# Kernel optimization log

Hardware: AMD Instinct MI355X
Metric: run time of the kernel (lower is better)

## Reference

```python
import jax, jax.numpy as jnp
import numpy as np

B, T, C, H = 1024, 256, 384, 64
NEG_INF = -1e30


def setup_inputs() -> dict:
    key = jax.random.key(0)
    kx, kk, kq, kv = jax.random.split(key, 4)
    return {
        "x": jax.random.normal(kx, (B, T, C), dtype=jnp.float32),
        "Wk": jax.random.normal(kk, (C, H), dtype=jnp.float32) * (C ** -0.5),
        "Wq": jax.random.normal(kq, (C, H), dtype=jnp.float32) * (C ** -0.5),
        "Wv": jax.random.normal(kv, (C, H), dtype=jnp.float32) * (C ** -0.5),
    }


def reference(x, Wk, Wq, Wv):
    # Single causal self-attention head (eval mode: dropout is identity).
    k = jnp.einsum("btc,ch->bth", x, Wk)  # [B,T,H]
    q = jnp.einsum("btc,ch->bth", x, Wq)
    v = jnp.einsum("btc,ch->bth", x, Wv)
    scale = jnp.asarray(k.shape[-1], x.dtype) ** -0.5
    w = jnp.einsum("bqh,bkh->bqk", q, k) * scale  # [B,T,T]
    Tn = x.shape[1]
    causal = jnp.tril(jnp.ones((Tn, Tn), dtype=bool))
    w = jnp.where(causal, w, NEG_INF)
    w = jax.nn.softmax(w, axis=-1)
    return jnp.einsum("bqk,bkh->bqh", w, v)  # [B,T,H]
```

## Files before the change

### kernel.cpp

```cpp
#include <hip/hip_runtime.h>

typedef __attribute__((ext_vector_type(8))) short short8;
typedef __attribute__((ext_vector_type(4))) float f32x4;

#define LDX 40
#define LDW 40
#define LDP 72

__device__ __forceinline__ ushort f2bf(float f) {
  unsigned u = __builtin_bit_cast(unsigned, f);
  u = (u + 0x7fffu + ((u >> 16) & 1u)) >> 16;
  return (ushort)u;
}

__global__ void prep_w(const float* __restrict__ Wk, const float* __restrict__ Wq,
                       const float* __restrict__ Wv, ushort* __restrict__ Wt) {
  int n = blockIdx.x;
  int c = threadIdx.x;
  const float* src = (n < 64) ? Wq : ((n < 128) ? Wk : Wv);
  int h = n & 63;
  Wt[n * 384 + c] = f2bf(src[c * 64 + h]);
}

__global__ __launch_bounds__(256) void qkv_gemm(const float* __restrict__ x,
    const ushort* __restrict__ Wt, ushort* __restrict__ qg,
    ushort* __restrict__ kg, ushort* __restrict__ vtg) {
  __shared__ ushort xs[128 * LDX];
  __shared__ ushort ws[192 * LDW];
  const int tid = threadIdx.x;
  const int wave = tid >> 6;
  const int lane = tid & 63;
  const int quad = lane >> 4;
  const int l16 = lane & 15;
  const long t0 = (long)blockIdx.x * 128;

  f32x4 acc[12][2];
#pragma unroll
  for (int i = 0; i < 12; ++i)
#pragma unroll
    for (int j = 0; j < 2; ++j) acc[i][j] = f32x4{0.f, 0.f, 0.f, 0.f};

  for (int c0 = 0; c0 < 384; c0 += 32) {
    __syncthreads();
#pragma unroll
    for (int i = 0; i < 4; ++i) {
      int idx = i * 256 + tid;
      int row = idx >> 3, c4 = idx & 7;
      float4 f = *(const float4*)(x + (t0 + row) * 384 + c0 + c4 * 4);
      ushort4 h;
      h.x = f2bf(f.x); h.y = f2bf(f.y); h.z = f2bf(f.z); h.w = f2bf(f.w);
      *(ushort4*)(&xs[row * LDX + c4 * 4]) = h;
    }
#pragma unroll
    for (int i = 0; i < 3; ++i) {
      int idx = i * 256 + tid;
      int n = idx >> 2, cc = idx & 3;
      uint4 d = *(const uint4*)(Wt + n * 384 + c0 + cc * 8);
      *(uint4*)(&ws[n * LDW + cc * 8]) = d;
    }
    __syncthreads();
    short8 bfr[2];
#pragma unroll
    for (int tt = 0; tt < 2; ++tt)
      bfr[tt] = *(const short8*)(&xs[(wave * 32 + tt * 16 + l16) * LDX + quad * 8]);
#pragma unroll
    for (int mt = 0; mt < 12; ++mt) {
      short8 a = *(const short8*)(&ws[(mt * 16 + l16) * LDW + quad * 8]);
      acc[mt][0] = __builtin_amdgcn_mfma_f32_16x16x32_bf16(a, bfr[0], acc[mt][0], 0, 0, 0);
      acc[mt][1] = __builtin_amdgcn_mfma_f32_16x16x32_bf16(a, bfr[1], acc[mt][1], 0, 0, 0);
    }
  }
#pragma unroll
  for (int mt = 0; mt < 12; ++mt) {
    const int sel = mt >> 2;
    const int hb = (mt & 3) * 16 + quad * 4;
#pragma unroll
    for (int tt = 0; tt < 2; ++tt) {
      long tg = t0 + wave * 32 + tt * 16 + l16;
      if (sel < 2) {
        ushort4 h;
        h.x = f2bf(acc[mt][tt][0]); h.y = f2bf(acc[mt][tt][1]);
        h.z = f2bf(acc[mt][tt][2]); h.w = f2bf(acc[mt][tt][3]);
        ushort* dst = (sel == 0 ? qg : kg) + tg * 64 + hb;
        *(ushort4*)dst = h;
      } else {
        long b = tg >> 8;
        int tb = (int)(tg & 255);
#pragma unroll
        for (int r = 0; r < 4; ++r)
          vtg[b * 16384 + (long)(hb + r) * 256 + tb] = f2bf(acc[mt][tt][r]);
      }
    }
  }
}

__global__ __launch_bounds__(64, 2) void attn(const ushort* __restrict__ qg,
    const ushort* __restrict__ kg, const ushort* __restrict__ vtg,
    float* __restrict__ out) {
  __shared__ ushort ps[16 * LDP];
  const int lane = threadIdx.x;
  const int quad = lane >> 4;
  const int l16 = lane & 15;
  const int qb = blockIdx.x;
  const int b = blockIdx.y;
  const long qbase = (long)b * 256 + qb * 64;

  short8 qf[4][2];
#pragma unroll
  for (int mt = 0; mt < 4; ++mt)
#pragma unroll
    for (int kk = 0; kk < 2; ++kk)
      qf[mt][kk] = *(const short8*)(qg + (qbase + mt * 16 + l16) * 64 + kk * 32 + quad * 8);

  f32x4 O[4][4];
  float m_s[4][4], l_s[4][4];
#pragma unroll
  for (int mt = 0; mt < 4; ++mt) {
#pragma unroll
    for (int ht = 0; ht < 4; ++ht) O[mt][ht] = f32x4{0.f, 0.f, 0.f, 0.f};
#pragma unroll
    for (int r = 0; r < 4; ++r) { m_s[mt][r] = -3.0e38f; l_s[mt][r] = 0.f; }
  }
  const float sc = 0.125f * 1.44269504088896f;

  for (int kb = 0; kb <= qb; ++kb) {
    const long kbase = (long)b * 256 + kb * 64;
    short8 kf[4][2];
#pragma unroll
    for (int nt = 0; nt < 4; ++nt)
#pragma unroll
      for (int kk = 0; kk < 2; ++kk)
        kf[nt][kk] = *(const short8*)(kg + (kbase + nt * 16 + l16) * 64 + kk * 32 + quad * 8);
    short8 vf[2][4];
#pragma unroll
    for (int kk = 0; kk < 2; ++kk)
#pragma unroll
      for (int ht = 0; ht < 4; ++ht)
        vf[kk][ht] = *(const short8*)(vtg + (long)b * 16384 + (ht * 16 + l16) * 256 +
                                      kb * 64 + kk * 32 + quad * 8);
    const bool diag = (kb == qb);
#pragma unroll
    for (int mt = 0; mt < 4; ++mt) {
      f32x4 S[4];
#pragma unroll
      for (int nt = 0; nt < 4; ++nt) {
        S[nt] = f32x4{0.f, 0.f, 0.f, 0.f};
#pragma unroll
        for (int kk = 0; kk < 2; ++kk)
          S[nt] = __builtin_amdgcn_mfma_f32_16x16x32_bf16(qf[mt][kk], kf[nt][kk], S[nt], 0, 0, 0);
      }
      float s2[4][4];
#pragma unroll
      for (int nt = 0; nt < 4; ++nt)
#pragma unroll
        for (int r = 0; r < 4; ++r) {
          float v = S[nt][r] * sc;
          if (diag && (nt * 16 + l16) > (mt * 16 + quad * 4 + r)) v = -1.0e30f;
          s2[nt][r] = v;
        }
      float mnew[4], alpha[4], rsum[4];
#pragma unroll
      for (int r = 0; r < 4; ++r)
        mnew[r] = fmaxf(fmaxf(s2[0][r], s2[1][r]), fmaxf(s2[2][r], s2[3][r]));
#pragma unroll
      for (int off = 8; off > 0; off >>= 1)
#pragma unroll
        for (int r = 0; r < 4; ++r)
          mnew[r] = fmaxf(mnew[r], __shfl_xor(mnew[r], off, 64));
#pragma unroll
      for (int r = 0; r < 4; ++r) {
        mnew[r] = fmaxf(mnew[r], m_s[mt][r]);
        alpha[r] = exp2f(m_s[mt][r] - mnew[r]);
        m_s[mt][r] = mnew[r];
        rsum[r] = 0.f;
      }
#pragma unroll
      for (int nt = 0; nt < 4; ++nt)
#pragma unroll
        for (int r = 0; r < 4; ++r) {
          float p = exp2f(s2[nt][r] - mnew[r]);
          rsum[r] += p;
          ps[(quad * 4 + r) * LDP + nt * 16 + l16] = f2bf(p);
        }
#pragma unroll
      for (int off = 8; off > 0; off >>= 1)
#pragma unroll
        for (int r = 0; r < 4; ++r)
          rsum[r] += __shfl_xor(rsum[r], off, 64);
#pragma unroll
      for (int r = 0; r < 4; ++r)
        l_s[mt][r] = l_s[mt][r] * alpha[r] + rsum[r];
      __syncthreads();
#pragma unroll
      for (int ht = 0; ht < 4; ++ht)
#pragma unroll
        for (int r = 0; r < 4; ++r) O[mt][ht][r] *= alpha[r];
      short8 aP[2];
#pragma unroll
      for (int kk = 0; kk < 2; ++kk)
        aP[kk] = *(const short8*)(&ps[l16 * LDP + kk * 32 + quad * 8]);
#pragma unroll
      for (int kk = 0; kk < 2; ++kk)
#pragma unroll
        for (int ht = 0; ht < 4; ++ht)
          O[mt][ht] = __builtin_amdgcn_mfma_f32_16x16x32_bf16(aP[kk], vf[kk][ht], O[mt][ht], 0, 0, 0);
      __syncthreads();
    }
  }
#pragma unroll
  for (int mt = 0; mt < 4; ++mt)
#pragma unroll
    for (int r = 0; r < 4; ++r) {
      float inv = 1.0f / l_s[mt][r];
      long row = qbase + mt * 16 + quad * 4 + r;
#pragma unroll
      for (int ht = 0; ht < 4; ++ht)
        out[row * 64 + ht * 16 + l16] = O[mt][ht][r] * inv;
    }
}

extern "C" void kernel_launch(void* const* d_in, const int* in_sizes, int n_in,
                              void* d_out, int out_size, void* d_ws, size_t ws_size,
                              hipStream_t stream) {
  const float* x  = (const float*)d_in[0];
  const float* Wk = (const float*)d_in[1];
  const float* Wq = (const float*)d_in[2];
  const float* Wv = (const float*)d_in[3];
  float* out = (float*)d_out;

  ushort* Wt  = (ushort*)d_ws;
  ushort* qg  = (ushort*)((char*)d_ws + (1 << 18));
  ushort* kg  = qg + 16777216;
  ushort* vtg = kg + 16777216;

  prep_w<<<dim3(192), dim3(384), 0, stream>>>(Wk, Wq, Wv, Wt);
  qkv_gemm<<<dim3(2048), dim3(256), 0, stream>>>(x, Wt, qg, kg, vtg);
  attn<<<dim3(4, 1024), dim3(64), 0, stream>>>(qg, kg, vtg, out);
}
```

Baseline: 644.0 us.

## Fuse QKV projection and causal attention into one per-batch kernel in LDS

Replaces the separate QKV GEMM and attention kernels with one kernel per batch element. It computes Q, K and V^T into shared memory and then runs attention from LDS, with each wave handling a balanced pair of 16-row query strips. This removes the global round trip for the bf16 Q/K/V intermediates and one kernel launch. It also register-prefetches the next x/W tile and skips fully masked score tiles. The cost is about 140KB of LDS per block, which limits occupancy, and a 512-thread block that serialises the GEMM and attention phases.

Measured after the change: 599.2 us. 7.0% less time.

```diff
diff --git a/kernel.cpp b/kernel.cpp
--- a/kernel.cpp
+++ b/kernel.cpp
@@ -5,7 +5,16 @@
 
 #define LDX 40
 #define LDW 40
+#define LDQ 72
+#define LDV 264
 #define LDP 72
+
+#define XS_OFF 0
+#define WS_OFF 10240
+#define Q_OFF  17920
+#define K_OFF  36352
+#define VT_OFF 54784
+#define SMEM_ELEMS 71680
 
 __device__ __forceinline__ ushort f2bf(float f) {
   unsigned u = __builtin_bit_cast(unsigned, f);
@@ -22,140 +31,149 @@
   Wt[n * 384 + c] = f2bf(src[c * 64 + h]);
 }
 
-__global__ __launch_bounds__(256) void qkv_gemm(const float* __restrict__ x,
-    const ushort* __restrict__ Wt, ushort* __restrict__ qg,
-    ushort* __restrict__ kg, ushort* __restrict__ vtg) {
-  __shared__ ushort xs[128 * LDX];
-  __shared__ ushort ws[192 * LDW];
+__global__ __launch_bounds__(512, 2) void fused(const float* __restrict__ x,
+    const ushort* __restrict__ Wt, float* __restrict__ out) {
+  __shared__ ushort sm[SMEM_ELEMS];
   const int tid = threadIdx.x;
   const int wave = tid >> 6;
   const int lane = tid & 63;
   const int quad = lane >> 4;
   const int l16 = lane & 15;
-  const long t0 = (long)blockIdx.x * 128;
-
-  f32x4 acc[12][2];
-#pragma unroll
-  for (int i = 0; i < 12; ++i)
-#pragma unroll
-    for (int j = 0; j < 2; ++j) acc[i][j] = f32x4{0.f, 0.f, 0.f, 0.f};
-
-  for (int c0 = 0; c0 < 384; c0 += 32) {
-    __syncthreads();
+  const int b = blockIdx.x;
+  const int wm = wave >> 2;
+  const int wn = wave & 3;
+
+  f32x4 acc[6][4];
+#pragma unroll
+  for (int i = 0; i < 6; ++i)
+#pragma unroll
+    for (int j = 0; j < 4; ++j) acc[i][j] = f32x4{0.f, 0.f, 0.f, 0.f};
+
+  const float* xb = x + (long)b * 98304;
+  int xrow[4], xc4[4];
+#pragma unroll
+  for (int i = 0; i < 4; ++i) { int idx = i * 512 + tid; xrow[i] = idx >> 3; xc4[i] = idx & 7; }
+  const int wn0 = tid >> 2, wc0 = tid & 3;
+  const int wn1 = (tid + 512) >> 2;
+
+  ushort4 xh[4];
+  uint4 w0, w1;
+
+  auto LOADX = [&](int c0) {
 #pragma unroll
     for (int i = 0; i < 4; ++i) {
-      int idx = i * 256 + tid;
-      int row = idx >> 3, c4 = idx & 7;
-      float4 f = *(const float4*)(x + (t0 + row) * 384 + c0 + c4 * 4);
+      float4 f = *(const float4*)(xb + xrow[i] * 384 + c0 + xc4[i] * 4);
       ushort4 h;
       h.x = f2bf(f.x); h.y = f2bf(f.y); h.z = f2bf(f.z); h.w = f2bf(f.w);
-      *(ushort4*)(&xs[row * LDX + c4 * 4]) = h;
-    }
-#pragma unroll
-    for (int i = 0; i < 3; ++i) {
-      int idx = i * 256 + tid;
-      int n = idx >> 2, cc = idx & 3;
-      uint4 d = *(const uint4*)(Wt + n * 384 + c0 + cc * 8);
-      *(uint4*)(&ws[n * LDW + cc * 8]) = d;
-    }
+      xh[i] = h;
+    }
+  };
+  auto LOADW = [&](int c0) {
+    w0 = *(const uint4*)(Wt + wn0 * 384 + c0 + wc0 * 8);
+    if (tid < 256) w1 = *(const uint4*)(Wt + wn1 * 384 + c0 + wc0 * 8);
+  };
+
+  LOADX(0); LOADW(0);
+  for (int t = 0; t < 12; ++t) {
     __syncthreads();
-    short8 bfr[2];
-#pragma unroll
-    for (int tt = 0; tt < 2; ++tt)
-      bfr[tt] = *(const short8*)(&xs[(wave * 32 + tt * 16 + l16) * LDX + quad * 8]);
-#pragma unroll
-    for (int mt = 0; mt < 12; ++mt) {
-      short8 a = *(const short8*)(&ws[(mt * 16 + l16) * LDW + quad * 8]);
-      acc[mt][0] = __builtin_amdgcn_mfma_f32_16x16x32_bf16(a, bfr[0], acc[mt][0], 0, 0, 0);
-      acc[mt][1] = __builtin_amdgcn_mfma_f32_16x16x32_bf16(a, bfr[1], acc[mt][1], 0, 0, 0);
+#pragma unroll
+    for (int i = 0; i < 4; ++i)
+      *(ushort4*)(&sm[XS_OFF + xrow[i] * LDX + xc4[i] * 4]) = xh[i];
+    *(uint4*)(&sm[WS_OFF + wn0 * LDW + wc0 * 8]) = w0;
+    if (tid < 256) *(uint4*)(&sm[WS_OFF + wn1 * LDW + wc0 * 8]) = w1;
+    __syncthreads();
+    if (t < 11) { LOADX((t + 1) * 32); LOADW((t + 1) * 32); }
+    short8 bf[4];
+#pragma unroll
+    for (int tt = 0; tt < 4; ++tt)
+      bf[tt] = *(const short8*)(&sm[XS_OFF + (wn * 64 + tt * 16 + l16) * LDX + quad * 8]);
+#pragma unroll
+    for (int mt = 0; mt < 6; ++mt) {
+      short8 a = *(const short8*)(&sm[WS_OFF + (wm * 96 + mt * 16 + l16) * LDW + quad * 8]);
+#pragma unroll
+      for (int tt = 0; tt < 4; ++tt)
+        acc[mt][tt] = __builtin_amdgcn_mfma_f32_16x16x32_bf16(a, bf[tt], acc[mt][tt], 0, 0, 0);
     }
   }
-#pragma unroll
-  for (int mt = 0; mt < 12; ++mt) {
-    const int sel = mt >> 2;
-    const int hb = (mt & 3) * 16 + quad * 4;
-#pragma unroll
-    for (int tt = 0; tt < 2; ++tt) {
-      long tg = t0 + wave * 32 + tt * 16 + l16;
-      if (sel < 2) {
+
+#pragma unroll
+  for (int mt = 0; mt < 6; ++mt) {
+    const int chb = wm * 96 + mt * 16 + quad * 4;
+#pragma unroll
+    for (int tt = 0; tt < 4; ++tt) {
+      const int tok = wn * 64 + tt * 16 + l16;
+      if (chb < 64) {
         ushort4 h;
         h.x = f2bf(acc[mt][tt][0]); h.y = f2bf(acc[mt][tt][1]);
         h.z = f2bf(acc[mt][tt][2]); h.w = f2bf(acc[mt][tt][3]);
-        ushort* dst = (sel == 0 ? qg : kg) + tg * 64 + hb;
-        *(ushort4*)dst = h;
+        *(ushort4*)(&sm[Q_OFF + tok * LDQ + chb]) = h;
+      } else if (chb < 128) {
+        ushort4 h;
+        h.x = f2bf(acc[mt][tt][0]); h.y = f2bf(acc[mt][tt][1]);
+        h.z = f2bf(acc[mt][tt][2]); h.w = f2bf(acc[mt][tt][3]);
+        *(ushort4*)(&sm[K_OFF + tok * LDQ + (chb - 64)]) = h;
       } else {
-        long b = tg >> 8;
-        int tb = (int)(tg & 255);
 #pragma unroll
         for (int r = 0; r < 4; ++r)
-          vtg[b * 16384 + (long)(hb + r) * 256 + tb] = f2bf(acc[mt][tt][r]);
+          sm[VT_OFF + (chb - 128 + r) * LDV + tok] = f2bf(acc[mt][tt][r]);
       }
     }
   }
-}
-
-__global__ __launch_bounds__(64, 2) void attn(const ushort* __restrict__ qg,
-    const ushort* __restrict__ kg, const ushort* __restrict__ vtg,
-    float* __restrict__ out) {
-  __shared__ ushort ps[16 * LDP];
-  const int lane = threadIdx.x;
-  const int quad = lane >> 4;
-  const int l16 = lane & 15;
-  const int qb = blockIdx.x;
-  const int b = blockIdx.y;
-  const long qbase = (long)b * 256 + qb * 64;
-
-  short8 qf[4][2];
-#pragma unroll
-  for (int mt = 0; mt < 4; ++mt)
+  __syncthreads();
+
+  const float sc = 0.125f * 1.44269504088896f;
+  ushort* psw = &sm[XS_OFF + wave * (16 * LDP)];
+
+  for (int si = 0; si < 2; ++si) {
+    const int strip = (si == 0) ? wave : (15 - wave);
+    const int qs = strip * 16;
+    const int nblk = strip;
+    const int lastkb = nblk >> 2;
+
+    short8 qf[2];
 #pragma unroll
     for (int kk = 0; kk < 2; ++kk)
-      qf[mt][kk] = *(const short8*)(qg + (qbase + mt * 16 + l16) * 64 + kk * 32 + quad * 8);
-
-  f32x4 O[4][4];
-  float m_s[4][4], l_s[4][4];
-#pragma unroll
-  for (int mt = 0; mt < 4; ++mt) {
-#pragma unroll
-    for (int ht = 0; ht < 4; ++ht) O[mt][ht] = f32x4{0.f, 0.f, 0.f, 0.f};
-#pragma unroll
-    for (int r = 0; r < 4; ++r) { m_s[mt][r] = -3.0e38f; l_s[mt][r] = 0.f; }
-  }
-  const float sc = 0.125f * 1.44269504088896f;
-
-  for (int kb = 0; kb <= qb; ++kb) {
-    const long kbase = (long)b * 256 + kb * 64;
-    short8 kf[4][2];
-#pragma unroll
-    for (int nt = 0; nt < 4; ++nt)
+      qf[kk] = *(const short8*)(&sm[Q_OFF + (qs + l16) * LDQ + kk * 32 + quad * 8]);
+
+    f32x4 O[4];
+    float ms[4], ls[4];
+#pragma unroll
+    for (int ht = 0; ht < 4; ++ht) O[ht] = f32x4{0.f, 0.f, 0.f, 0.f};
+#pragma unroll
+    for (int r = 0; r < 4; ++r) { ms[r] = -3.0e38f; ls[r] = 0.f; }
+
+    for (int kb = 0; kb <= lastkb; ++kb) {
+      short8 kf[4][2], vf[2][4];
+#pragma unroll
+      for (int nt = 0; nt < 4; ++nt)
+#pragma unroll
+        for (int kk = 0; kk < 2; ++kk)
+          kf[nt][kk] = *(const short8*)(&sm[K_OFF + (kb * 64 + nt * 16 + l16) * LDQ + kk * 32 + quad * 8]);
 #pragma unroll
       for (int kk = 0; kk < 2; ++kk)
-        kf[nt][kk] = *(const short8*)(kg + (kbase + nt * 16 + l16) * 64 + kk * 32 + quad * 8);
-    short8 vf[2][4];
-#pragma unroll
-    for (int kk = 0; kk < 2; ++kk)
-#pragma unroll
-      for (int ht = 0; ht < 4; ++ht)
-        vf[kk][ht] = *(const short8*)(vtg + (long)b * 16384 + (ht * 16 + l16) * 256 +
-                                      kb * 64 + kk * 32 + quad * 8);
-    const bool diag = (kb == qb);
-#pragma unroll
-    for (int mt = 0; mt < 4; ++mt) {
+#pragma unroll
+        for (int ht = 0; ht < 4; ++ht)
+          vf[kk][ht] = *(const short8*)(&sm[VT_OFF + (ht * 16 + l16) * LDV + kb * 64 + kk * 32 + quad * 8]);
+
+      const int gmax = nblk - kb * 4;
       f32x4 S[4];
 #pragma unroll
       for (int nt = 0; nt < 4; ++nt) {
         S[nt] = f32x4{0.f, 0.f, 0.f, 0.f};
-#pragma unroll
-        for (int kk = 0; kk < 2; ++kk)
-          S[nt] = __builtin_amdgcn_mfma_f32_16x16x32_bf16(qf[mt][kk], kf[nt][kk], S[nt], 0, 0, 0);
+        if (nt <= gmax) {
+#pragma unroll
+          for (int kk = 0; kk < 2; ++kk)
+            S[nt] = __builtin_amdgcn_mfma_f32_16x16x32_bf16(qf[kk], kf[nt][kk], S[nt], 0, 0, 0);
+        }
       }
+      const bool lastg = (kb == lastkb);
       float s2[4][4];
 #pragma unroll
       for (int nt = 0; nt < 4; ++nt)
 #pragma unroll
         for (int r = 0; r < 4; ++r) {
           float v = S[nt][r] * sc;
-          if (diag && (nt * 16 + l16) > (mt * 16 + quad * 4 + r)) v = -1.0e30f;
+          if (lastg && (kb * 64 + nt * 16 + l16) > (qs + quad * 4 + r)) v = -1.0e30f;
           s2[nt][r] = v;
         }
       float mnew[4], alpha[4], rsum[4];
@@ -169,9 +187,9 @@
           mnew[r] = fmaxf(mnew[r], __shfl_xor(mnew[r], off, 64));
 #pragma unroll
       for (int r = 0; r < 4; ++r) {
-        mnew[r] = fmaxf(mnew[r], m_s[mt][r]);
-        alpha[r] = exp2f(m_s[mt][r] - mnew[r]);
-        m_s[mt][r] = mnew[r];
+        mnew[r] = fmaxf(mnew[r], ms[r]);
+        alpha[r] = exp2f(ms[r] - mnew[r]);
+        ms[r] = mnew[r];
         rsum[r] = 0.f;
       }
 #pragma unroll
@@ -180,7 +198,7 @@
         for (int r = 0; r < 4; ++r) {
           float p = exp2f(s2[nt][r] - mnew[r]);
           rsum[r] += p;
-          ps[(quad * 4 + r) * LDP + nt * 16 + l16] = f2bf(p);
+          psw[(quad * 4 + r) * LDP + nt * 16 + l16] = f2bf(p);
         }
 #pragma unroll
       for (int off = 8; off > 0; off >>= 1)
@@ -189,34 +207,32 @@
           rsum[r] += __shfl_xor(rsum[r], off, 64);
 #pragma unroll
       for (int r = 0; r < 4; ++r)
-        l_s[mt][r] = l_s[mt][r] * alpha[r] + rsum[r];
-      __syncthreads();
+        ls[r] = ls[r] * alpha[r] + rsum[r];
+      asm volatile("s_waitcnt lgkmcnt(0)" ::: "memory");
+      __builtin_amdgcn_sched_barrier(0);
 #pragma unroll
       for (int ht = 0; ht < 4; ++ht)
 #pragma unroll
-        for (int r = 0; r < 4; ++r) O[mt][ht][r] *= alpha[r];
+        for (int r = 0; r < 4; ++r) O[ht][r] *= alpha[r];
       short8 aP[2];
 #pragma unroll
       for (int kk = 0; kk < 2; ++kk)
-        aP[kk] = *(const short8*)(&ps[l16 * LDP + kk * 32 + quad * 8]);
+        aP[kk] = *(const short8*)(&psw[l16 * LDP + kk * 32 + quad * 8]);
 #pragma unroll
       for (int kk = 0; kk < 2; ++kk)
 #pragma unroll
         for (int ht = 0; ht < 4; ++ht)
-          O[mt][ht] = __builtin_amdgcn_mfma_f32_16x16x32_bf16(aP[kk], vf[kk][ht], O[mt][ht], 0, 0, 0);
-      __syncthreads();
+          O[ht] = __builtin_amdgcn_mfma_f32_16x16x32_bf16(aP[kk], vf[kk][ht], O[ht], 0, 0, 0);
+    }
+#pragma unroll
+    for (int r = 0; r < 4; ++r) {
+      float inv = 1.0f / ls[r];
+      long row = (long)b * 256 + qs + quad * 4 + r;
+#pragma unroll
+      for (int ht = 0; ht < 4; ++ht)
+        out[row * 64 + ht * 16 + l16] = O[ht][r] * inv;
     }
   }
-#pragma unroll
-  for (int mt = 0; mt < 4; ++mt)
-#pragma unroll
-    for (int r = 0; r < 4; ++r) {
-      float inv = 1.0f / l_s[mt][r];
-      long row = qbase + mt * 16 + quad * 4 + r;
-#pragma unroll
-      for (int ht = 0; ht < 4; ++ht)
-        out[row * 64 + ht * 16 + l16] = O[mt][ht][r] * inv;
-    }
 }
 
 extern "C" void kernel_launch(void* const* d_in, const int* in_sizes, int n_in,
@@ -228,12 +244,8 @@
   const float* Wv = (const float*)d_in[3];
   float* out = (float*)d_out;
 
-  ushort* Wt  = (ushort*)d_ws;
-  ushort* qg  = (ushort*)((char*)d_ws + (1 << 18));
-  ushort* kg  = qg + 16777216;
-  ushort* vtg = kg + 16777216;
+  ushort* Wt = (ushort*)d_ws;
 
   prep_w<<<dim3(192), dim3(384), 0, stream>>>(Wk, Wq, Wv, Wt);
-  qkv_gemm<<<dim3(2048), dim3(256), 0, stream>>>(x, Wt, qg, kg, vtg);
-  attn<<<dim3(4, 1024), dim3(64), 0, stream>>>(qg, kg, vtg, out);
-}
+  fused<<<dim3(1024), dim3(512), 0, stream>>>(x, Wt, out);
+}
```
